# Kernel optimization log

Hardware: AMD Instinct MI355X
Metric: run time of the kernel (lower is better)

Reference implementation:

```python
import jax, jax.numpy as jnp
import numpy as np

N = 100000
E = 1600000
F_IN = 256
H1, C1 = 4, 32          # layer 1: heads=4, out_channels=32, concat=True -> 128
H2, C2 = 1, 16          # layer 2: heads=1, out_channels=nclass=16, concat=False
SLOPE = 0.2             # leaky relu negative slope


def setup_inputs() -> dict:
    key = jax.random.key(0)
    ks = jax.random.split(key, 10)
    x = jax.random.normal(ks[0], (N, F_IN), dtype=jnp.float32)
    row = jax.random.randint(ks[1], (E,), 0, N, dtype=jnp.int32)      # source j
    off = jax.random.randint(ks[2], (E,), 1, N, dtype=jnp.int32)
    col = ((row + off) % N).astype(jnp.int32)                          # target i, no self loops
    edge_index = jnp.stack([row, col])

    def glorot(k, shape, fan_in, fan_out):
        lim = np.sqrt(6.0 / (fan_in + fan_out))
        return jax.random.uniform(k, shape, jnp.float32, -lim, lim)

    W1 = glorot(ks[3], (F_IN, H1 * C1), F_IN, H1 * C1)
    att1 = glorot(ks[4], (1, H1, 2 * C1), H1, 2 * C1)
    b1 = jnp.zeros((H1 * C1,), jnp.float32)
    W2 = glorot(ks[5], (H1 * C1, H2 * C2), H1 * C1, H2 * C2)
    att2 = glorot(ks[6], (1, H2, 2 * C2), H2, 2 * C2)
    b2 = jnp.zeros((C2,), jnp.float32)
    return {"x": x, "edge_index": edge_index, "W1": W1, "att1": att1,
            "b1": b1, "W2": W2, "att2": att2, "b2": b2}


def gcn_norm(edge_index, num_nodes):
    # add_remaining_self_loops + symmetric normalization (GeoLayer.norm)
    loop = jnp.arange(num_nodes, dtype=edge_index.dtype)
    row = jnp.concatenate([edge_index[0], loop])
    col = jnp.concatenate([edge_index[1], loop])
    w = jnp.ones(row.shape[0], jnp.float32)
    deg = jax.ops.segment_sum(w, row, num_segments=num_nodes)
    dinv = jnp.where(deg > 0, jax.lax.rsqrt(deg), 0.0)
    return row, col, dinv[row] * w * dinv[col]


def segment_softmax(alpha, seg, num_segments):
    amax = jax.ops.segment_max(alpha, seg, num_segments=num_segments)
    ex = jnp.exp(alpha - amax[seg])
    denom = jax.ops.segment_sum(ex, seg, num_segments=num_segments)
    return ex / (denom[seg] + 1e-16)


def geo_layer(x, row, col, ew, W, att, b, heads, out_ch, concat):
    n = x.shape[0]
    xt = (x @ W).reshape(n, heads, out_ch)
    x_i = xt[col]                         # [E+N, H, C] target features
    x_j = xt[row]                         # [E+N, H, C] source features
    wl, wr = att[:, :, :out_ch], att[:, :, out_ch:]
    # (cat([x_i,x_j],-1) * att).sum(-1) == (x_i*wl).sum + (x_j*wr).sum
    alpha = (x_i * wl).sum(-1) + (x_j * wr).sum(-1)     # [E+N, H]
    alpha = jnp.where(alpha >= 0, alpha, SLOPE * alpha)  # leaky_relu
    alpha = segment_softmax(alpha, col, n)
    msg = ew[:, None, None] * x_j * alpha[:, :, None]    # [E+N, H, C]
    out = jax.ops.segment_sum(msg, col, num_segments=n)  # scatter-add to targets
    out = out.reshape(n, heads * out_ch) if concat else out.mean(axis=1)
    return out + b


def reference(x, edge_index, W1, att1, b1, W2, att2, b2):
    # norm is identical for both layers (edge_weight=None each time)
    row, col, ew = gcn_norm(edge_index, x.shape[0])
    h = geo_layer(x, row, col, ew, W1, att1, b1, H1, C1, True)
    h = jax.nn.relu(h)
    out = geo_layer(h, row, col, ew, W2, att2, b2, H2, C2, False)
    return out
```

## Files before the change

kernel.cpp:

```cpp
#include <hip/hip_runtime.h>
#include <math.h>

#define TPB 256
#define SEGN 512
#define SCAP 14336
#define CHB 8192
#define CAPC 12288

__device__ __forceinline__ float lrelu(float a){ return a >= 0.f ? a : 0.2f*a; }

typedef __attribute__((ext_vector_type(8))) short bf16x8;
typedef __attribute__((ext_vector_type(4))) float f32x4;

__device__ __forceinline__ unsigned short bfr(float f){
  unsigned u = __float_as_uint(f);
  return (unsigned short)((u + 0x7fffu + ((u >> 16) & 1u)) >> 16);
}

__device__ __forceinline__ void gl_lds16(const void* g, void* l){
  __builtin_amdgcn_global_load_lds(
      (const __attribute__((address_space(1))) void*)g,
      (__attribute__((address_space(3))) void*)l, 16, 0, 0);
}


__global__ __launch_bounds__(256) void k_bucketM(const int* __restrict__ rows, const int* __restrict__ cols,
    int* __restrict__ bcurC, int* __restrict__ bcurR,
    unsigned* __restrict__ ebufC, unsigned short* __restrict__ ebufR, int E, int NSEG2){
  __shared__ int lhC[256], lbC[256], lhR[256], lbR[256];
  int tid = threadIdx.x;
  int e0 = blockIdx.x * CHB;
  #pragma unroll 1
  for(int r=0; r<4; r++){
    lhC[tid] = 0; lhR[tid] = 0;
    __syncthreads();
    int eb = e0 + r*2048;
    unsigned pk[8]; int sgC[8], rkC[8], sgR[8], rkR[8]; int pvR[8];
    #pragma unroll
    for(int i=0;i<8;i++){
      int e = eb + i*256 + tid;
      sgC[i] = -1;
      if(e < E){
        int cc = cols[e], rr = rows[e];
        sgC[i] = cc >> 9;
        pk[i]  = ((unsigned)(cc & (SEGN-1)) << 17) | (unsigned)rr;
        rkC[i] = atomicAdd(&lhC[sgC[i]], 1);
        sgR[i] = rr >> 9;
        pvR[i] = rr & (SEGN-1);
        rkR[i] = atomicAdd(&lhR[sgR[i]], 1);
      }
    }
    __syncthreads();
    if(tid < NSEG2){
      int c = lhC[tid];  lbC[tid] = c  ? atomicAdd(&bcurC[tid], c)  : 0;
      int c2 = lhR[tid]; lbR[tid] = c2 ? atomicAdd(&bcurR[tid], c2) : 0;
    }
    __syncthreads();
    #pragma unroll
    for(int i=0;i<8;i++)
      if(sgC[i] >= 0){
        int p = lbC[sgC[i]] + rkC[i];
        if(p < CAPC) ebufC[sgC[i]*CAPC + p] = pk[i];
        int p2 = lbR[sgR[i]] + rkR[i];
        if(p2 < CAPC) ebufR[sgR[i]*CAPC + p2] = (unsigned short)pvR[i];
      }
    __syncthreads();
  }
}

__global__ __launch_bounds__(256) void k_cntseg(const int* __restrict__ bcurC, const int* __restrict__ bcurR,
    const unsigned* __restrict__ ebufC, const unsigned short* __restrict__ ebufR,
    int* __restrict__ cnt, float* __restrict__ dinv, int* __restrict__ bsum, int N){
  __shared__ int hc[SEGN];
  __shared__ int hr[SEGN];
  __shared__ int red[256];
  int s = blockIdx.x, tid = threadIdx.x;
  int lo = s*SEGN;
  int nn = min(SEGN, N - lo);
  for(int i=tid; i<SEGN; i+=256){ hc[i] = 0; hr[i] = 0; }
  __syncthreads();
  int cb = s*CAPC;
  int cc = min(bcurC[s], CAPC);
  int rc = min(bcurR[s], CAPC);
  for(int j=tid; j<cc; j+=256) atomicAdd(&hc[ebufC[cb + j] >> 17], 1);
  for(int j=tid; j<rc; j+=256) atomicAdd(&hr[ebufR[cb + j]], 1);
  __syncthreads();
  int tsum = 0;
  for(int i=tid; i<nn; i+=256){
    int c = hc[i] + 1;
    cnt[lo+i]  = c;
    tsum += c;
    dinv[lo+i] = 1.f / sqrtf((float)(hr[i] + 1));
  }
  red[tid] = tsum; __syncthreads();
  for(int off=128; off>0; off>>=1){
    if(tid < off) red[tid] += red[tid+off];
    __syncthreads();
  }
  if(tid == 0) bsum[s] = red[0];
}

__global__ void k_scan_bsum(int* bsum, int NB){
  __shared__ int s[256];
  int t = threadIdx.x;
  int v = (t < NB) ? bsum[t] : 0;
  s[t] = v; __syncthreads();
  for(int off=1; off<256; off<<=1){
    int add = (t >= off) ? s[t-off] : 0;
    __syncthreads();
    s[t] += add;
    __syncthreads();
  }
  if(t < NB) bsum[t] = s[t] - v;
}

__global__ __launch_bounds__(256) void k_sortfill2(const int* __restrict__ cnt,
    const int* __restrict__ bsum, const int* __restrict__ bcurC,
    const unsigned* __restrict__ ebuf, int* __restrict__ offs,
    int* __restrict__ csr, int N){
  __shared__ int lcur[SEGN];
  __shared__ int lbuf[SCAP];
  __shared__ int sdata[256];
  int s = blockIdx.x, tid = threadIdx.x;
  int lo = s*SEGN;
  int nn = min(SEGN, N - lo);
  int base = bsum[s];
  int i0 = tid*2, i1 = i0+1;
  int v0 = (i0 < nn) ? cnt[lo+i0] : 0;
  int v1 = (i1 < nn) ? cnt[lo+i1] : 0;
  int ssum = v0 + v1;
  sdata[tid] = ssum; __syncthreads();
  int mine = ssum;
  for(int off=1; off<256; off<<=1){
    int add = (tid >= off) ? sdata[tid-off] : 0;
    __syncthreads();
    sdata[tid] += add;
    __syncthreads();
  }
  int total = sdata[255];
  int run0 = sdata[tid] - mine;
  int run1 = run0 + v0;
  int eb = s*CAPC;
  int ec = min(bcurC[s], CAPC);
  if(total <= SCAP){
    if(i0 < nn){
      offs[lo+i0] = base + run0;
      lbuf[run0]  = lo + i0;
      lcur[i0]    = run0 + 1;
      if(lo+i0 == N-1) offs[N] = base + run0 + v0;
    }
    if(i1 < nn){
      offs[lo+i1] = base + run1;
      lbuf[run1]  = lo + i1;
      lcur[i1]    = run1 + 1;
      if(lo+i1 == N-1) offs[N] = base + run1 + v1;
    }
    __syncthreads();
    for(int j=tid; j<ec; j+=256){
      unsigned pk = ebuf[eb + j];
      int li  = pk >> 17;
      int row = pk & 0x1FFFF;
      int p = atomicAdd(&lcur[li], 1);
      lbuf[p] = row;
    }
    __syncthreads();
    for(int j=tid; j<total; j+=256) csr[base + j] = lbuf[j];
  } else {
    if(i0 < nn){
      offs[lo+i0] = base + run0;
      csr[base+run0] = lo + i0;
      lcur[i0] = base + run0 + 1;
      if(lo+i0 == N-1) offs[N] = base + run0 + v0;
    }
    if(i1 < nn){
      offs[lo+i1] = base + run1;
      csr[base+run1] = lo + i1;
      lcur[i1] = base + run1 + 1;
      if(lo+i1 == N-1) offs[N] = base + run1 + v1;
    }
    __syncthreads();
    for(int j=tid; j<ec; j+=256){
      unsigned pk = ebuf[eb + j];
      int li  = pk >> 17;
      int row = pk & 0x1FFFF;
      int p = atomicAdd(&lcur[li], 1);
      csr[p] = row;
    }
  }
}


__global__ void k_prepW(const float* __restrict__ W, short* __restrict__ Whi,
                        short* __restrict__ Wlo){
  int idx = blockIdx.x*256 + threadIdx.x;
  int n = idx >> 8, k = idx & 255;
  float f = W[k*128 + n];
  unsigned short h = bfr(f);
  float hf = __uint_as_float(((unsigned)h) << 16);
  Whi[n*256 + k] = (short)h;
  Wlo[n*256 + k] = (short)bfr(f - hf);
}


#define BUFB 24576
__global__ __launch_bounds__(256) void k_gemm1(
    const float* __restrict__ x,
    const short* __restrict__ Whi, const short* __restrict__ Wlo,
    const float* __restrict__ att1,
    unsigned* __restrict__ xtb, float* __restrict__ sl, float* __restrict__ sr, int N){
  __shared__ __align__(16) char smem[2*BUFB];
  float* fx = (float*)smem;
  float* att_sh = (float*)(smem + 17408);

  int tid = threadIdx.x;
  int n0 = blockIdx.x * 64;
  int w = tid >> 6, l = tid & 63;
  int wm = w & 1, wn = w >> 1;
  int lm = l & 15, lq = l >> 4;

  f32x4 acc[2][4];
  #pragma unroll
  for(int a=0;a<2;a++)
    #pragma unroll
    for(int b=0;b<4;b++) acc[a][b] = (f32x4){0.f,0.f,0.f,0.f};

  int ua0 = (w<<6) | l, ua1 = 256 + ua0;
  int ar0 = ua0 >> 3, as0 = (ua0 & 7) ^ (ar0 & 7);
  int ar1 = ua1 >> 3, as1 = (ua1 & 7) ^ (ar1 & 7);
  const float* gA0 = x + (size_t)min(n0 + ar0, N-1)*256 + as0*4;
  const float* gA1 = x + (size_t)min(n0 + ar1, N-1)*256 + as1*4;
  int ub0 = (w<<6) | l,  ub1 = 256 + ub0;
  int br0 = ub0 >> 2, bs0 = (ub0 & 3) ^ ((br0 >> 1) & 3);
  int br1 = ub1 >> 2, bs1 = (ub1 & 3) ^ ((br1 >> 1) & 3);
  const short* gBh0 = Whi + br0*256 + bs0*8;
  const short* gBh1 = Whi + br1*256 + bs1*8;
  const short* gBl0 = Wlo + br0*256 + bs0*8;
  const short* gBl1 = Wlo + br1*256 + bs1*8;
  int woff = w << 10;

  int offAf[2][2], offB[4];
  #pragma unroll
  for(int mt=0;mt<2;mt++){
    int rr = wm*32 + mt*16 + lm;
    offAf[mt][0] = rr*32 + (((2*lq+0) ^ (rr&7)) << 2);
    offAf[mt][1] = rr*32 + (((2*lq+1) ^ (rr&7)) << 2);
  }
  #pragma unroll
  for(int nt=0;nt<4;nt++){
    int rr = wn*64 + nt*16 + lm;
    offB[nt] = rr*32 + ((lq ^ ((rr>>1)&3)) << 3);
  }

  {
    char* base = smem;
    gl_lds16(gA0,  base          + woff);
    gl_lds16(gA1,  base + 4096   + woff);
    gl_lds16(gBh0, base + 8192   + woff);
    gl_lds16(gBh1, base + 12288  + woff);
    gl_lds16(gBl0, base + 16384  + woff);
    gl_lds16(gBl1, base + 20480  + woff);
  }
  __syncthreads();

  int cur = 0;
  #pragma unroll 1
  for(int c=0;c<8;c++){
    if(c < 7){
      int kf = (c+1) << 5;
      char* base = smem + (cur^1)*BUFB;
      gl_lds16(gA0  + kf, base          + woff);
      gl_lds16(gA1  + kf, base + 4096   + woff);
      gl_lds16(gBh0 + kf, base + 8192   + woff);
      gl_lds16(gBh1 + kf, base + 12288  + woff);
      gl_lds16(gBl0 + kf, base + 16384  + woff);
      gl_lds16(gBl1 + kf, base + 20480  + woff);
    }
    float* Axf = (float*)(smem + cur*BUFB);
    short* Bh  = (short*)(smem + cur*BUFB + 8192);
    short* Bl  = (short*)(smem + cur*BUFB + 16384);
    bf16x8 ah[2], al2[2];
    #pragma unroll
    for(int mt=0;mt<2;mt++){
      float4 f0 = *((const float4*)&Axf[offAf[mt][0]]);
      float4 f1 = *((const float4*)&Axf[offAf[mt][1]]);
      float fa[8] = {f0.x,f0.y,f0.z,f0.w,f1.x,f1.y,f1.z,f1.w};
      #pragma unroll
      for(int j=0;j<8;j++){
        unsigned short hb = bfr(fa[j]);
        float hf = __uint_as_float(((unsigned)hb) << 16);
        ah[mt][j]  = (short)hb;
        al2[mt][j] = (short)bfr(fa[j] - hf);
      }
    }
    #pragma unroll
    for(int nt=0;nt<4;nt++){
      bf16x8 bh = *((bf16x8*)&Bh[offB[nt]]);
      bf16x8 bl = *((bf16x8*)&Bl[offB[nt]]);
      #pragma unroll
      for(int mt=0;mt<2;mt++){
        acc[mt][nt] = __builtin_amdgcn_mfma_f32_16x16x32_bf16(ah[mt],  bh, acc[mt][nt], 0,0,0);
        acc[mt][nt] = __builtin_amdgcn_mfma_f32_16x16x32_bf16(ah[mt],  bl, acc[mt][nt], 0,0,0);
        acc[mt][nt] = __builtin_amdgcn_mfma_f32_16x16x32_bf16(al2[mt], bh, acc[mt][nt], 0,0,0);
      }
    }
    __syncthreads();
    cur ^= 1;
  }

  #pragma unroll
  for(int mt=0;mt<2;mt++){
    #pragma unroll
    for(int v=0;v<4;v++){
      int row = n0 + wm*32 + mt*16 + lq*4 + v;
      if(row < N){
        unsigned p0 = (unsigned)bfr(acc[mt][0][v]) | ((unsigned)bfr(acc[mt][2][v])<<16);
        unsigned p1 = (unsigned)bfr(acc[mt][1][v]) | ((unsigned)bfr(acc[mt][3][v])<<16);
        int jb = wn*32 + lm;
        xtb[(size_t)row*64 + jb]      = p0;
        xtb[(size_t)row*64 + jb + 16] = p1;
      }
    }
  }

  att_sh[tid] = att1[tid];
  #pragma unroll 1
  for(int p=0;p<2;p++){
    __syncthreads();
    if(wn == p){
      #pragma unroll
      for(int mt=0;mt<2;mt++)
        #pragma unroll
        for(int nt=0;nt<4;nt++)
          #pragma unroll
          for(int v=0;v<4;v++)
            fx[(wm*32 + mt*16 + lq*4 + v)*68 + nt*16 + lm] = acc[mt][nt][v];
    }
    __syncthreads();
    if(tid < 128){
      int rloc = tid >> 1, hh = tid & 1;
      int head = p*2 + hh;
      float a = 0.f, b = 0.f;
      #pragma unroll
      for(int c4=0;c4<8;c4++){
        float4 xv  = *((const float4*)&fx[rloc*68 + hh*32 + c4*4]);
        float4 alv = *((const float4*)&att_sh[head*64 + c4*4]);
        float4 arv = *((const float4*)&att_sh[head*64 + 32 + c4*4]);
        a += xv.x*alv.x + xv.y*alv.y + xv.z*alv.z + xv.w*alv.w;
        b += xv.x*arv.x + xv.y*arv.y + xv.z*arv.z + xv.w*arv.w;
      }
      int row = n0 + rloc;
      if(row < N){
        sl[(size_t)row*4 + head] = a;
        sr[(size_t)row*4 + head] = b;
      }
    }
  }
}


__global__ __launch_bounds__(64) void k_agg1(const int* __restrict__ offs, const int* __restrict__ srcs,
    const float* __restrict__ sl, const float* __restrict__ sr, const float* __restrict__ dinv,
    const unsigned* __restrict__ xtb, const float* __restrict__ b1,
    const float* __restrict__ W2, const float* __restrict__ att2,
    float* __restrict__ sl2, float* __restrict__ sr2, unsigned* __restrict__ xt2b, int N){
  __shared__ int   s_sh[64];
  __shared__ float w_sh[64*4];
  __shared__ float h_sh[144];
  int n = blockIdx.x;
  if(n >= N) return;
  int lane = threadIdx.x;
  int beg = offs[n], end = offs[n+1];
  int deg = end - beg;
  float4 sln = *((const float4*)(sl + (size_t)n*4));
  int h0 = lane >> 5;
  float den0=0.f,den1=0.f,den2=0.f,den3=0.f;
  float acc0=0.f, acc1=0.f;

  if(deg <= 64){
    int j = beg + lane;
    int s = 0; float wd = 0.f;
    float a0=-1e30f, a1=-1e30f, a2=-1e30f, a3=-1e30f;
    if(j < end){
      s = srcs[j];
      float4 a = *((const float4*)(sr + (size_t)s*4));
      a0 = lrelu(sln.x + a.x);
      a1 = lrelu(sln.y + a.y);
      a2 = lrelu(sln.z + a.z);
      a3 = lrelu(sln.w + a.w);
      wd = dinv[s];
    }
    float m0=a0,m1=a1,m2=a2,m3=a3;
    #pragma unroll
    for(int o=32;o>0;o>>=1){
      m0 = fmaxf(m0, __shfl_xor(m0,o));
      m1 = fmaxf(m1, __shfl_xor(m1,o));
      m2 = fmaxf(m2, __shfl_xor(m2,o));
      m3 = fmaxf(m3, __shfl_xor(m3,o));
    }
    den0 = __expf(a0 - m0);
    den1 = __expf(a1 - m1);
    den2 = __expf(a2 - m2);
    den3 = __expf(a3 - m3);
    s_sh[lane] = s;
    w_sh[lane*4+0] = wd*den0;
    w_sh[lane*4+1] = wd*den1;
    w_sh[lane*4+2] = wd*den2;
    w_sh[lane*4+3] = wd*den3;
    __syncthreads();
    int k = 0;
    for(; k+8<=deg; k+=8){
      int sk[8];
      #pragma unroll
      for(int u=0;u<8;u++) sk[u] = __builtin_amdgcn_readfirstlane(s_sh[k+u]);
      unsigned pv[8];
      #pragma unroll
      for(int u=0;u<8;u++) pv[u] = xtb[(size_t)sk[u]*64 + lane];
      #pragma unroll
      for(int u=0;u<8;u++){
        float2 wv = *((const float2*)&w_sh[(k+u)*4 + h0*2]);
        acc0 += wv.x * __uint_as_float(pv[u] << 16);
        acc1 += wv.y * __uint_as_float(pv[u] & 0xffff0000u);
      }
    }
    for(; k<deg; k++){
      int sk = __builtin_amdgcn_readfirstlane(s_sh[k]);
      unsigned pvv = xtb[(size_t)sk*64 + lane];
      float2 wv = *((const float2*)&w_sh[k*4 + h0*2]);
      acc0 += wv.x * __uint_as_float(pvv << 16);
      acc1 += wv.y * __uint_as_float(pvv & 0xffff0000u);
    }
  } else {
    float m0=-1e30f,m1=-1e30f,m2=-1e30f,m3=-1e30f;
    for(int j=beg+lane; j<end; j+=64){
      int s = srcs[j];
      float4 a = *((const float4*)(sr + (size_t)s*4));
      m0 = fmaxf(m0, lrelu(sln.x + a.x));
      m1 = fmaxf(m1, lrelu(sln.y + a.y));
      m2 = fmaxf(m2, lrelu(sln.z + a.z));
      m3 = fmaxf(m3, lrelu(sln.w + a.w));
    }
    #pragma unroll
    for(int o=32;o>0;o>>=1){
      m0 = fmaxf(m0, __shfl_xor(m0,o));
      m1 = fmaxf(m1, __shfl_xor(m1,o));
      m2 = fmaxf(m2, __shfl_xor(m2,o));
      m3 = fmaxf(m3, __shfl_xor(m3,o));
    }
    for(int c0=beg; c0<end; c0+=64){
      int cnt = min(64, end-c0);
      int j = c0 + lane;
      float e0=0.f,e1=0.f,e2=0.f,e3=0.f, wd=0.f; int s=0;
      if(j<end){
        s = srcs[j];
        float4 a = *((const float4*)(sr + (size_t)s*4));
        e0 = __expf(lrelu(sln.x + a.x) - m0);
        e1 = __expf(lrelu(sln.y + a.y) - m1);
        e2 = __expf(lrelu(sln.z + a.z) - m2);
        e3 = __expf(lrelu(sln.w + a.w) - m3);
        wd = dinv[s];
      }
      den0+=e0; den1+=e1; den2+=e2; den3+=e3;
      s_sh[lane] = s;
      w_sh[lane*4+0] = wd*e0;
      w_sh[lane*4+1] = wd*e1;
      w_sh[lane*4+2] = wd*e2;
      w_sh[lane*4+3] = wd*e3;
      __syncthreads();
      int k = 0;
      for(; k+8<=cnt; k+=8){
        int sk[8];
        #pragma unroll
        for(int u=0;u<8;u++) sk[u] = __builtin_amdgcn_readfirstlane(s_sh[k+u]);
        unsigned pv[8];
        #pragma unroll
        for(int u=0;u<8;u++) pv[u] = xtb[(size_t)sk[u]*64 + lane];
        #pragma unroll
        for(int u=0;u<8;u++){
          float2 wv = *((const float2*)&w_sh[(k+u)*4 + h0*2]);
          acc0 += wv.x * __uint_as_float(pv[u] << 16);
          acc1 += wv.y * __uint_as_float(pv[u] & 0xffff0000u);
        }
      }
      for(; k<cnt; k++){
        int sk = __builtin_amdgcn_readfirstlane(s_sh[k]);
        unsigned pvv = xtb[(size_t)sk*64 + lane];
        float2 wv = *((const float2*)&w_sh[k*4 + h0*2]);
        acc0 += wv.x * __uint_as_float(pvv << 16);
        acc1 += wv.y * __uint_as_float(pvv & 0xffff0000u);
      }
      __syncthreads();
    }
  }
  #pragma unroll
  for(int o=32;o>0;o>>=1){
    den0 += __shfl_xor(den0,o);
    den1 += __shfl_xor(den1,o);
    den2 += __shfl_xor(den2,o);
    den3 += __shfl_xor(den3,o);
  }
  float din = dinv[n];
  int ch0 = (lane < 32) ? lane : lane + 32;
  int ch1 = ch0 + 32;
  float d0 = (lane < 32) ? den0 : den2;
  float d1 = (lane < 32) ? den1 : den3;
  float o0 = din*acc0/(d0 + 1e-16f) + b1[ch0];
  float o1 = din*acc1/(d1 + 1e-16f) + b1[ch1];
  o0 = o0 > 0.f ? o0 : 0.f;
  o1 = o1 > 0.f ? o1 : 0.f;

  h_sh[ch0] = o0;
  h_sh[ch1] = o1;
  __syncthreads();
  int c4 = lane & 3, q = lane >> 2;
  const float4* W24 = (const float4*)W2;
  f32x4 a4 = (f32x4){0.f,0.f,0.f,0.f};
  #pragma unroll
  for(int j=0;j<8;j++){
    int k = q*8 + j;
    float hv = h_sh[k];
    float4 wv = W24[k*4 + c4];
    a4[0] += hv*wv.x; a4[1] += hv*wv.y; a4[2] += hv*wv.z; a4[3] += hv*wv.w;
  }
  #pragma unroll
  for(int o=4;o<64;o<<=1){
    a4[0] += __shfl_xor(a4[0],o);
    a4[1] += __shfl_xor(a4[1],o);
    a4[2] += __shfl_xor(a4[2],o);
    a4[3] += __shfl_xor(a4[3],o);
  }
  if(lane < 4){
    h_sh[128 + lane*4 + 0] = a4[0];
    h_sh[128 + lane*4 + 1] = a4[1];
    h_sh[128 + lane*4 + 2] = a4[2];
    h_sh[128 + lane*4 + 3] = a4[3];
  }
  __syncthreads();
  if(lane < 16){
    float v = h_sh[128 + lane];
    float t0 = v*att2[lane], t1 = v*att2[16 + lane];
    #pragma unroll
    for(int o=1;o<16;o<<=1){ t0 += __shfl_xor(t0,o); t1 += __shfl_xor(t1,o); }
    if(lane == 0){ sl2[n] = t0; sr2[n] = t1; }
  }
  if(lane < 8){
    unsigned pk = (unsigned)bfr(h_sh[128+lane]) | ((unsigned)bfr(h_sh[128+lane+8])<<16);
    xt2b[(size_t)n*8 + lane] = pk;
  }
}


__global__ __launch_bounds__(64) void k_agg2(const int* __restrict__ offs, const int* __restrict__ srcs,
    const float* __restrict__ sl2, const float* __restrict__ sr2, const float* __restrict__ dinv,
    const unsigned* __restrict__ xt2b, const float* __restrict__ b2, float* __restrict__ out, int N){
  __shared__ int   s_sh[64];
  __shared__ float w_sh[64];
  int n = blockIdx.x;
  if(n >= N) return;
  int lane = threadIdx.x;
  int beg = offs[n], end = offs[n+1];
  int deg = end - beg;
  float sln = sl2[n];
  float den = 0.f, acc0 = 0.f, acc1 = 0.f;
  int grp = lane >> 3, ch = lane & 7;

  if(deg <= 64){
    int j = beg + lane;
    int s = 0; float wd = 0.f; float a = -1e30f;
    if(j < end){
      s = srcs[j];
      a = lrelu(sln + sr2[s]);
      wd = dinv[s];
    }
    float m = a;
    #pragma unroll
    for(int o=32;o>0;o>>=1) m = fmaxf(m, __shfl_xor(m,o));
    float e = __expf(a - m);
    den = e;
    s_sh[lane] = s;
    w_sh[lane] = wd*e;
    __syncthreads();
    for(int k=0;k<deg;k+=8){
      int kk = k + grp;
      if(kk < deg){
        int sk = s_sh[kk];
        float wk = w_sh[kk];
        unsigned pv = xt2b[(size_t)sk*8 + ch];
        acc0 += wk * __uint_as_float(pv << 16);
        acc1 += wk * __uint_as_float(pv & 0xffff0000u);
      }
    }
  } else {
    float m = -1e30f;
    for(int j=beg+lane; j<end; j+=64)
      m = fmaxf(m, lrelu(sln + sr2[srcs[j]]));
    #pragma unroll
    for(int o=32;o>0;o>>=1) m = fmaxf(m, __shfl_xor(m,o));
    for(int c0=beg; c0<end; c0+=64){
      int cnt = min(64, end-c0);
      int j = c0 + lane;
      float e=0.f, wd=0.f; int s=0;
      if(j<end){
        s = srcs[j];
        e = __expf(lrelu(sln + sr2[s]) - m);
        wd = dinv[s];
      }
      den += e;
      s_sh[lane] = s;
      w_sh[lane] = wd*e;
      __syncthreads();
      for(int k=0;k<cnt;k+=8){
        int kk = k + grp;
        if(kk < cnt){
          int sk = s_sh[kk];
          float wk = w_sh[kk];
          unsigned pv = xt2b[(size_t)sk*8 + ch];
          acc0 += wk * __uint_as_float(pv << 16);
          acc1 += wk * __uint_as_float(pv & 0xffff0000u);
        }
      }
      __syncthreads();
    }
  }
  #pragma unroll
  for(int o=32;o>0;o>>=1) den += __shfl_xor(den,o);
  acc0 += __shfl_xor(acc0,8);  acc0 += __shfl_xor(acc0,16);  acc0 += __shfl_xor(acc0,32);
  acc1 += __shfl_xor(acc1,8);  acc1 += __shfl_xor(acc1,16);  acc1 += __shfl_xor(acc1,32);
  if(lane < 8){
    float din = dinv[n];
    out[(size_t)n*16 + lane]     = din*acc0/(den + 1e-16f) + b2[lane];
    out[(size_t)n*16 + lane + 8] = din*acc1/(den + 1e-16f) + b2[lane+8];
  }
}


extern "C" void kernel_launch(void* const* d_in, const int* in_sizes, int n_in,
                              void* d_out, int out_size, void* d_ws, size_t ws_size,
                              hipStream_t stream){
  const float* x    = (const float*)d_in[0];
  const int*   ei   = (const int*)d_in[1];
  const float* W1   = (const float*)d_in[2];
  const float* att1 = (const float*)d_in[3];
  const float* b1   = (const float*)d_in[4];
  const float* W2   = (const float*)d_in[5];
  const float* att2 = (const float*)d_in[6];
  const float* b2   = (const float*)d_in[7];
  int N = in_sizes[0] / 256;
  int E = in_sizes[1] / 2;
  const int* rows = ei;
  const int* cols = ei + E;
  float* out = (float*)d_out;

  int ET    = E + N;
  int NSEG2 = (N + SEGN - 1) / SEGN;

  char* p = (char*)d_ws;
  auto alloc = [&](size_t bytes)->void*{ void* q = p; p += (bytes + 255) & ~(size_t)255; return q; };
  int*      cnt     = (int*)alloc((size_t)N*4);
  int*      offs    = (int*)alloc((size_t)(N+1)*4);
  int*      bsum    = (int*)alloc(256*4);
  int*      bcur    = (int*)alloc(512*4);
  int*      csr     = (int*)alloc((size_t)ET*4);
  float*    dinv    = (float*)alloc((size_t)N*4);
  unsigned* xtb     = (unsigned*)alloc((size_t)N*64*4);
  float*    sl1     = (float*)alloc((size_t)N*16);
  float*    sr1     = (float*)alloc((size_t)N*16);
  unsigned* xt2b    = (unsigned*)alloc((size_t)N*8*4);
  float*    sl2     = (float*)alloc((size_t)N*4);
  float*    sr2     = (float*)alloc((size_t)N*4);
  short*    Whi     = (short*)alloc((size_t)128*256*2);
  short*    Wlo     = (short*)alloc((size_t)128*256*2);

  int* bcurC = bcur;
  int* bcurR = bcur + 256;

  unsigned*       ebufC = (unsigned*)xtb;
  unsigned short* ebufR = (unsigned short*)(ebufC + (size_t)NSEG2*CAPC);

  int gB = (E + CHB - 1) / CHB;

  hipMemsetAsync(bcur, 0, 512*4, stream);
  k_bucketM<<<gB, 256, 0, stream>>>(rows, cols, bcurC, bcurR, ebufC, ebufR, E, NSEG2);
  k_cntseg<<<NSEG2, 256, 0, stream>>>(bcurC, bcurR, ebufC, ebufR, cnt, dinv, bsum, N);
  k_scan_bsum<<<1, 256, 0, stream>>>(bsum, NSEG2);
  k_sortfill2<<<NSEG2, 256, 0, stream>>>(cnt, bsum, bcurC, ebufC, offs, csr, N);

  k_prepW<<<128, 256, 0, stream>>>(W1, Whi, Wlo);
  k_gemm1<<<(N + 63)/64, 256, 0, stream>>>(x, Whi, Wlo, att1, xtb, sl1, sr1, N);
  k_agg1<<<N, 64, 0, stream>>>(offs, csr, sl1, sr1, dinv, xtb, b1, W2, att2, sl2, sr2, xt2b, N);
  k_agg2<<<N, 64, 0, stream>>>(offs, csr, sl2, sr2, dinv, xt2b, b2, out, N);
}
```

Measured before the change: 406.4 us.

## Split layer-2 projection out of agg1 into a separate tiled GEMM kernel

```diff
diff --git a/kernel.cpp b/kernel.cpp
--- a/kernel.cpp
+++ b/kernel.cpp
@@ -360,12 +360,9 @@
 
 __global__ __launch_bounds__(64) void k_agg1(const int* __restrict__ offs, const int* __restrict__ srcs,
     const float* __restrict__ sl, const float* __restrict__ sr, const float* __restrict__ dinv,
-    const unsigned* __restrict__ xtb, const float* __restrict__ b1,
-    const float* __restrict__ W2, const float* __restrict__ att2,
-    float* __restrict__ sl2, float* __restrict__ sr2, unsigned* __restrict__ xt2b, int N){
+    const unsigned* __restrict__ xtb, const float* __restrict__ b1, float* __restrict__ h, int N){
   __shared__ int   s_sh[64];
   __shared__ float w_sh[64*4];
-  __shared__ float h_sh[144];
   int n = blockIdx.x;
   if(n >= N) return;
   int lane = threadIdx.x;
@@ -505,46 +502,57 @@
   float d1 = (lane < 32) ? den1 : den3;
   float o0 = din*acc0/(d0 + 1e-16f) + b1[ch0];
   float o1 = din*acc1/(d1 + 1e-16f) + b1[ch1];
-  o0 = o0 > 0.f ? o0 : 0.f;
-  o1 = o1 > 0.f ? o1 : 0.f;
-
-  h_sh[ch0] = o0;
-  h_sh[ch1] = o1;
+  h[(size_t)n*128 + ch0] = o0 > 0.f ? o0 : 0.f;
+  h[(size_t)n*128 + ch1] = o1 > 0.f ? o1 : 0.f;
+}
+
+
+__global__ __launch_bounds__(256) void k_gemm2(const float* __restrict__ hmat, const float* __restrict__ W2,
+    const float* __restrict__ att2, unsigned* __restrict__ xt2b,
+    float* __restrict__ sl2, float* __restrict__ sr2, int N){
+  __shared__ float hs[16*132];
+  __shared__ float ws[16*132];
+  __shared__ float xs[16*16];
+  int t = threadIdx.x;
+  int n0 = blockIdx.x * 16;
+  #pragma unroll
+  for(int i=0;i<8;i++){
+    int idx = t + 256*i;
+    int k = idx >> 4, c = idx & 15;
+    ws[c*132 + k] = W2[idx];
+  }
+  #pragma unroll
+  for(int i=0;i<2;i++){
+    int idx = t + 256*i;
+    int r = idx >> 5, k4 = idx & 31;
+    int n = n0 + r;
+    float4 v = make_float4(0.f,0.f,0.f,0.f);
+    if(n < N) v = ((const float4*)hmat)[(size_t)n*32 + k4];
+    *((float4*)&hs[r*132 + k4*4]) = v;
+  }
   __syncthreads();
-  int c4 = lane & 3, q = lane >> 2;
-  const float4* W24 = (const float4*)W2;
-  f32x4 a4 = (f32x4){0.f,0.f,0.f,0.f};
-  #pragma unroll
-  for(int j=0;j<8;j++){
-    int k = q*8 + j;
-    float hv = h_sh[k];
-    float4 wv = W24[k*4 + c4];
-    a4[0] += hv*wv.x; a4[1] += hv*wv.y; a4[2] += hv*wv.z; a4[3] += hv*wv.w;
-  }
-  #pragma unroll
-  for(int o=4;o<64;o<<=1){
-    a4[0] += __shfl_xor(a4[0],o);
-    a4[1] += __shfl_xor(a4[1],o);
-    a4[2] += __shfl_xor(a4[2],o);
-    a4[3] += __shfl_xor(a4[3],o);
-  }
-  if(lane < 4){
-    h_sh[128 + lane*4 + 0] = a4[0];
-    h_sh[128 + lane*4 + 1] = a4[1];
-    h_sh[128 + lane*4 + 2] = a4[2];
-    h_sh[128 + lane*4 + 3] = a4[3];
-  }
+  int r = t >> 4, c = t & 15;
+  float acc = 0.f;
+  for(int k=0;k<128;k+=4){
+    float4 hv = *((const float4*)&hs[r*132+k]);
+    float4 wv = *((const float4*)&ws[c*132+k]);
+    acc += hv.x*wv.x + hv.y*wv.y + hv.z*wv.z + hv.w*wv.w;
+  }
+  xs[r*16 + c] = acc;
   __syncthreads();
-  if(lane < 16){
-    float v = h_sh[128 + lane];
-    float t0 = v*att2[lane], t1 = v*att2[16 + lane];
-    #pragma unroll
-    for(int o=1;o<16;o<<=1){ t0 += __shfl_xor(t0,o); t1 += __shfl_xor(t1,o); }
-    if(lane == 0){ sl2[n] = t0; sr2[n] = t1; }
-  }
-  if(lane < 8){
-    unsigned pk = (unsigned)bfr(h_sh[128+lane]) | ((unsigned)bfr(h_sh[128+lane+8])<<16);
-    xt2b[(size_t)n*8 + lane] = pk;
+  int n = n0 + r;
+  if(c < 8 && n < N){
+    unsigned pk = (unsigned)bfr(xs[r*16+c]) | ((unsigned)bfr(xs[r*16+c+8])<<16);
+    xt2b[(size_t)n*8 + c] = pk;
+  }
+  if(t < 16){
+    int nn = n0 + t;
+    if(nn < N){
+      float a = 0.f, b = 0.f;
+      #pragma unroll
+      for(int cc=0;cc<16;cc++){ float v = xs[t*16+cc]; a += v*att2[cc]; b += v*att2[16+cc]; }
+      sl2[nn] = a; sr2[nn] = b;
+    }
   }
 }
 
@@ -664,6 +672,7 @@
   unsigned* xtb     = (unsigned*)alloc((size_t)N*64*4);
   float*    sl1     = (float*)alloc((size_t)N*16);
   float*    sr1     = (float*)alloc((size_t)N*16);
+  float*    hbuf    = (float*)alloc((size_t)N*128*4);
   unsigned* xt2b    = (unsigned*)alloc((size_t)N*8*4);
   float*    sl2     = (float*)alloc((size_t)N*4);
   float*    sr2     = (float*)alloc((size_t)N*4);
@@ -686,6 +695,8 @@
 
   k_prepW<<<128, 256, 0, stream>>>(W1, Whi, Wlo);
   k_gemm1<<<(N + 63)/64, 256, 0, stream>>>(x, Whi, Wlo, att1, xtb, sl1, sr1, N);
-  k_agg1<<<N, 64, 0, stream>>>(offs, csr, sl1, sr1, dinv, xtb, b1, W2, att2, sl2, sr2, xt2b, N);
+  k_agg1<<<N, 64, 0, stream>>>(offs, csr, sl1, sr1, dinv, xtb, b1, hbuf, N);
+
+  k_gemm2<<<(N + 15)/16, 256, 0, stream>>>(hbuf, W2, att2, xt2b, sl2, sr2, N);
   k_agg2<<<N, 64, 0, stream>>>(offs, csr, sl2, sr2, dinv, xt2b, b2, out, N);
 }
```

New measurement: 406.4 us. About the same (-0.0%).
